# Kernel optimization log

Hardware: AMD Instinct MI355X
Metric: run time of the kernel (lower is better)

The kernel has to match this reference:

```python
import jax, jax.numpy as jnp
import numpy as np

D_MODEL = 16   # output feature dim of channel_proj
D_STATE = 8    # Mamba SSM state size
D_CONV = 2     # causal depthwise conv kernel size
D_INNER = 4    # expand * mamba_d_model = 2 * 2
DT_RANK = 1    # ceil(mamba_d_model / 16)


def setup_inputs() -> dict:
    key = jax.random.key(0)
    ks = jax.random.split(key, 10)
    B, W, P, T = 8, 16, 36, 2048
    s = 0.1
    raw_signals = jax.random.normal(ks[0], (B, W, P, 2, T), jnp.float32)
    in_proj_w = jax.random.normal(ks[1], (2 * D_INNER, 2), jnp.float32) * s
    conv_w = jax.random.normal(ks[2], (D_INNER, D_CONV), jnp.float32) * s
    conv_b = jax.random.normal(ks[3], (D_INNER,), jnp.float32) * s
    x_proj_w = jax.random.normal(ks[4], (DT_RANK + 2 * D_STATE, D_INNER), jnp.float32) * s
    dt_proj_w = jax.random.normal(ks[5], (D_INNER, DT_RANK), jnp.float32) * s
    dt_proj_b = jax.random.normal(ks[6], (D_INNER,), jnp.float32) * s
    # Standard S4D-real init: A_log = log(1..d_state) per inner channel
    A_log = jnp.log(jnp.tile(jnp.arange(1, D_STATE + 1, dtype=jnp.float32), (D_INNER, 1)))
    D_skip = jnp.ones((D_INNER,), jnp.float32)
    out_proj_w = jax.random.normal(ks[7], (2, D_INNER), jnp.float32) * s
    proj_w = jax.random.normal(ks[8], (D_MODEL, 2), jnp.float32) * s
    proj_b = jax.random.normal(ks[9], (D_MODEL,), jnp.float32) * s
    return dict(raw_signals=raw_signals, in_proj_w=in_proj_w, conv_w=conv_w,
                conv_b=conv_b, x_proj_w=x_proj_w, dt_proj_w=dt_proj_w,
                dt_proj_b=dt_proj_b, A_log=A_log, D_skip=D_skip,
                out_proj_w=out_proj_w, proj_w=proj_w, proj_b=proj_b)


def _mamba(u, in_proj_w, conv_w, conv_b, x_proj_w, dt_proj_w, dt_proj_b,
           A_log, D_skip, out_proj_w):
    # u: [N, L, 2] -> [N, L, 2]
    N, L, _ = u.shape
    xz = u @ in_proj_w.T                               # [N, L, 2*D_INNER]
    x, z = jnp.split(xz, 2, axis=-1)                   # each [N, L, D_INNER]
    # causal depthwise conv1d (kernel D_CONV, left-padded)
    xp = jnp.pad(x, ((0, 0), (D_CONV - 1, 0), (0, 0)))
    xc = sum(xp[:, k:k + L, :] * conv_w[:, k] for k in range(D_CONV)) + conv_b
    x = jax.nn.silu(xc)
    x_dbl = x @ x_proj_w.T                             # [N, L, DT_RANK + 2*D_STATE]
    dt, Bs, Cs = jnp.split(x_dbl, [DT_RANK, DT_RANK + D_STATE], axis=-1)
    dt = jax.nn.softplus(dt @ dt_proj_w.T + dt_proj_b)  # [N, L, D_INNER]
    A = -jnp.exp(A_log)                                # [D_INNER, D_STATE]

    def step(h, inp):
        dt_t, B_t, x_t, C_t = inp                      # [N,d], [N,s], [N,d], [N,s]
        dA = jnp.exp(dt_t[:, :, None] * A)             # [N, d, s]
        h = dA * h + (dt_t * x_t)[:, :, None] * B_t[:, None, :]
        y = jnp.einsum('nds,ns->nd', h, C_t)
        return h, y

    h0 = jnp.zeros((N, D_INNER, D_STATE), u.dtype)
    xs = (dt.transpose(1, 0, 2), Bs.transpose(1, 0, 2),
          x.transpose(1, 0, 2), Cs.transpose(1, 0, 2))
    _, ys = jax.lax.scan(step, h0, xs)                 # ys: [L, N, D_INNER]
    y = ys.transpose(1, 0, 2) + x * D_skip
    y = y * jax.nn.silu(z)
    return y @ out_proj_w.T                            # [N, L, 2]


def reference(raw_signals, in_proj_w, conv_w, conv_b, x_proj_w, dt_proj_w,
              dt_proj_b, A_log, D_skip, out_proj_w, proj_w, proj_b):
    B, W, P, C, T = raw_signals.shape
    # permute(0,1,3,2) per window + reshape(-1, T, C): all windows batched at once
    u = raw_signals.transpose(0, 1, 2, 4, 3).reshape(B * W * P, T, C)
    y = _mamba(u, in_proj_w, conv_w, conv_b, x_proj_w, dt_proj_w, dt_proj_b,
               A_log, D_skip, out_proj_w)              # [BWP, T, 2]
    feat = y.mean(axis=1)                              # [BWP, 2]
    proj = jax.nn.relu(feat @ proj_w.T + proj_b)       # [BWP, D_MODEL] (dropout=eval no-op)
    out = proj.reshape(B, W, P, D_MODEL).mean(axis=2)  # aggregate_internal=True
    return out                                         # [B, W, D_MODEL]
```

## Files before the change

kernel.cpp:

```cpp
#include <hip/hip_runtime.h>


#define T_LEN  2048
#define N_SEQ  4608
#define SPB    2
#define TC     32
#define NCH    (T_LEN / TC)
#define LOG2E  1.4426950408889634f
#define LN2    0.6931471805599453f

__device__ __forceinline__ float fexp2(float x){ return __builtin_amdgcn_exp2f(x); }
__device__ __forceinline__ float frcp (float x){ return __builtin_amdgcn_rcpf(x); }
__device__ __forceinline__ float flog2(float x){ return __builtin_amdgcn_logf(x); }
__device__ __forceinline__ float silu_f(float v){ return v * frcp(1.0f + fexp2(v * -LOG2E)); }

__global__ __launch_bounds__(64, 4) void mamba_feat_kernel(
    const float* __restrict__ raw,
    const float* __restrict__ in_proj_w,
    const float* __restrict__ conv_w,
    const float* __restrict__ conv_b,
    const float* __restrict__ x_proj_w,
    const float* __restrict__ dt_proj_w,
    const float* __restrict__ dt_proj_b,
    const float* __restrict__ A_log,
    const float* __restrict__ D_skip,
    const float* __restrict__ out_proj_w,
    float* __restrict__ feat)
{
    __shared__ __attribute__((aligned(16))) float rec[SPB * TC * 32];

    const int j   = threadIdx.x;
    const int seq = j >> 5;
    const int tt  = j & 31;
    const int d2  = (j & 31) >> 3;
    const int s2  = j & 7;

    float wi[8][2];
#pragma unroll
    for (int r = 0; r < 8; ++r){ wi[r][0] = in_proj_w[r*2]; wi[r][1] = in_proj_w[r*2+1]; }
    float cw0[4], cw1[4], cb[4], dtw[4], dtb[4], op0[4], op1[4], op0D[4], op1D[4];
#pragma unroll
    for (int d = 0; d < 4; ++d){
        cw0[d] = conv_w[d*2]; cw1[d] = conv_w[d*2+1]; cb[d] = conv_b[d];
        dtw[d] = dt_proj_w[d]; dtb[d] = dt_proj_b[d];
        op0[d] = out_proj_w[d]; op1[d] = out_proj_w[4+d];
        float Dk = D_skip[d];
        op0D[d] = op0[d] * Dk; op1D[d] = op1[d] * Dk;
    }
    float xw[17][4];
#pragma unroll
    for (int r = 0; r < 17; ++r)
#pragma unroll
        for (int d = 0; d < 4; ++d) xw[r][d] = x_proj_w[r*4 + d];
    const float A2l = -fexp2(A_log[d2*8 + s2] * LOG2E) * LOG2E;

    const int n = blockIdx.x * SPB + seq;
    const float* u0base = raw + (size_t)n * 2 * T_LEN;
    const float* u1base = u0base + T_LEN;

    const int sbase = seq * (TC * 32);
    const int sl_dt = d2 >> 1,        in_dt = (d2 & 1) * 2;
    const int sl_bc = 2 + (s2 >> 1),  in_bc = (s2 & 1) * 2;
    int odt[8], obc[8], og[8];
#pragma unroll
    for (int k2 = 0; k2 < 8; ++k2){
        odt[k2] = sbase + ((sl_dt ^ k2) << 2) + in_dt;
        obc[k2] = sbase + ((sl_bc ^ k2) << 2) + in_bc;
        og [k2] = sbase + ((6     ^ k2) << 2) + d2;
    }

    float h = 0.f, q = 0.f, sk0 = 0.f, sk1 = 0.f;

    float cu0 = u0base[tt], cu1 = u1base[tt];
    float pu0 = (tt > 0) ? u0base[tt-1] : 0.f;
    float pu1 = (tt > 0) ? u1base[tt-1] : 0.f;
    float nu0 = 0.f, nu1 = 0.f, np0 = 0.f, np1 = 0.f;

    for (int c = 0; c < NCH; ++c){
        float x[4], g[4];
#pragma unroll
        for (int d = 0; d < 4; ++d){
            float xr = fmaf(cu0, wi[d][0],   cu1 * wi[d][1]);
            float xp = fmaf(pu0, wi[d][0],   pu1 * wi[d][1]);
            float zr = fmaf(cu0, wi[4+d][0], cu1 * wi[4+d][1]);
            float xc = fmaf(xp, cw0[d], fmaf(xr, cw1[d], cb[d]));
            x[d] = silu_f(xc);
            g[d] = silu_f(zr);
        }
        float dtr = 0.f;
#pragma unroll
        for (int d = 0; d < 4; ++d) dtr = fmaf(x[d], xw[0][d], dtr);
        float Bv[8], Cv[8];
#pragma unroll
        for (int s = 0; s < 8; ++s){
            float b  = x[0] * xw[1+s][0];
            float cc = x[0] * xw[9+s][0];
#pragma unroll
            for (int d = 1; d < 4; ++d){
                b  = fmaf(x[d], xw[1+s][d], b);
                cc = fmaf(x[d], xw[9+s][d], cc);
            }
            Bv[s] = b; Cv[s] = cc;
        }
        float dt[4], dtx[4];
#pragma unroll
        for (int d = 0; d < 4; ++d){
            float v = fmaf(dtr, dtw[d], dtb[d]);
            dt[d]  = LN2 * flog2(1.0f + fexp2(v * LOG2E));
            dtx[d] = dt[d] * x[d];
        }
#pragma unroll
        for (int d = 0; d < 4; ++d){
            float gx = g[d] * x[d];
            sk0 = fmaf(gx, op0D[d], sk0);
            sk1 = fmaf(gx, op1D[d], sk1);
        }
        {
            const int rb = seq*(TC*32) + tt*32;
            const int tk = tt & 7;
            *(float4*)&rec[rb + ((0^tk)<<2)] = make_float4(dt[0], dtx[0], dt[1], dtx[1]);
            *(float4*)&rec[rb + ((1^tk)<<2)] = make_float4(dt[2], dtx[2], dt[3], dtx[3]);
            *(float4*)&rec[rb + ((2^tk)<<2)] = make_float4(Bv[0], Cv[0], Bv[1], Cv[1]);
            *(float4*)&rec[rb + ((3^tk)<<2)] = make_float4(Bv[2], Cv[2], Bv[3], Cv[3]);
            *(float4*)&rec[rb + ((4^tk)<<2)] = make_float4(Bv[4], Cv[4], Bv[5], Cv[5]);
            *(float4*)&rec[rb + ((5^tk)<<2)] = make_float4(Bv[6], Cv[6], Bv[7], Cv[7]);
            *(float4*)&rec[rb + ((6^tk)<<2)] = make_float4(g[0], g[1], g[2], g[3]);
        }
        __syncthreads();

        if (c + 1 < NCH){
            const int t = (c+1)*TC + tt;
            nu0 = u0base[t];   nu1 = u1base[t];
            np0 = u0base[t-1]; np1 = u1base[t-1];
        }

#pragma unroll
        for (int st = 0; st < TC; ++st){
            const int k2 = st & 7;
            const int tb = st * 32;
            const float2 ddx = *(const float2*)&rec[tb + odt[k2]];
            const float2 bc  = *(const float2*)&rec[tb + obc[k2]];
            const float  gt  = rec[tb + og[k2]];
            const float dA = fexp2(ddx.x * A2l);
            h = fmaf(dA, h, ddx.y * bc.x);
            q = fmaf(h, bc.y * gt, q);
        }
        __syncthreads();

        cu0 = nu0; cu1 = nu1; pu0 = np0; pu1 = np1;
    }

    float v0 = fmaf(q, op0[d2], sk0);
    float v1 = fmaf(q, op1[d2], sk1);
#pragma unroll
    for (int m = 16; m >= 1; m >>= 1){
        v0 += __shfl_xor(v0, m, 64);
        v1 += __shfl_xor(v1, m, 64);
    }
    if ((j & 31) == 0){
        feat[(size_t)n*2    ] = v0 * (1.0f / T_LEN);
        feat[(size_t)n*2 + 1] = v1 * (1.0f / T_LEN);
    }
}

__global__ void proj_kernel(const float* __restrict__ feat,
                            const float* __restrict__ pw,
                            const float* __restrict__ pb,
                            float* __restrict__ out)
{
    const int tid = blockIdx.x * blockDim.x + threadIdx.x;
    const int grp = tid >> 4;
    const int m   = tid & 15;
    const float w0 = pw[m*2], w1 = pw[m*2+1], b = pb[m];
    const float* f = feat + (size_t)grp * 36 * 2;
    float acc = 0.f;
#pragma unroll
    for (int p = 0; p < 36; ++p){
        float v = fmaf(f[p*2], w0, fmaf(f[p*2+1], w1, b));
        acc += fmaxf(v, 0.f);
    }
    out[tid] = acc * (1.0f / 36.0f);
}

extern "C" void kernel_launch(void* const* d_in, const int* in_sizes, int n_in,
                              void* d_out, int out_size, void* d_ws, size_t ws_size,
                              hipStream_t stream)
{
    (void)in_sizes; (void)n_in; (void)out_size; (void)ws_size;
    const float* raw        = (const float*)d_in[0];
    const float* in_proj_w  = (const float*)d_in[1];
    const float* conv_w     = (const float*)d_in[2];
    const float* conv_b     = (const float*)d_in[3];
    const float* x_proj_w   = (const float*)d_in[4];
    const float* dt_proj_w  = (const float*)d_in[5];
    const float* dt_proj_b  = (const float*)d_in[6];
    const float* A_log      = (const float*)d_in[7];
    const float* D_skip     = (const float*)d_in[8];
    const float* out_proj_w = (const float*)d_in[9];
    const float* proj_w     = (const float*)d_in[10];
    const float* proj_b     = (const float*)d_in[11];

    float* feat = (float*)d_ws;

    mamba_feat_kernel<<<dim3(N_SEQ / SPB), dim3(64), 0, stream>>>(
        raw, in_proj_w, conv_w, conv_b, x_proj_w, dt_proj_w, dt_proj_b,
        A_log, D_skip, out_proj_w, feat);

    proj_kernel<<<dim3(8), dim3(256), 0, stream>>>(feat, proj_w, proj_b, (float*)d_out);
}
```

Baseline: 161.3 us.

## Split the sequence scan into two time halves with a linear-recurrence combine

The per-sequence selective scan is split across two blocks along time. The second half runs from a zero state and also accumulates the cumulative decay product weighted by C*gate, so its missing contribution from the first half's final state can be added afterwards. A new combine kernel merges the partial sums, which doubles the grid and shortens each block's serial chain. The second half does extra multiplies per step, and the change adds a kernel launch plus workspace traffic.

```diff
diff --git a/kernel.cpp b/kernel.cpp
--- a/kernel.cpp
+++ b/kernel.cpp
@@ -5,7 +5,9 @@
 #define N_SEQ  4608
 #define SPB    2
 #define TC     32
-#define NCH    (T_LEN / TC)
+#define TSPLIT 2
+#define TH     (T_LEN / TSPLIT)
+#define NCHH   (TH / TC)
 #define LOG2E  1.4426950408889634f
 #define LN2    0.6931471805599453f
 
@@ -14,7 +16,7 @@
 __device__ __forceinline__ float flog2(float x){ return __builtin_amdgcn_logf(x); }
 __device__ __forceinline__ float silu_f(float v){ return v * frcp(1.0f + fexp2(v * -LOG2E)); }
 
-__global__ __launch_bounds__(64, 4) void mamba_feat_kernel(
+__global__ __launch_bounds__(64, 4) void mamba_half_kernel(
     const float* __restrict__ raw,
     const float* __restrict__ in_proj_w,
     const float* __restrict__ conv_w,
@@ -25,15 +27,19 @@
     const float* __restrict__ A_log,
     const float* __restrict__ D_skip,
     const float* __restrict__ out_proj_w,
-    float* __restrict__ feat)
+    float* __restrict__ H0,
+    float* __restrict__ W1,
+    float* __restrict__ QR)
 {
     __shared__ __attribute__((aligned(16))) float rec[SPB * TC * 32];
 
-    const int j   = threadIdx.x;
-    const int seq = j >> 5;
-    const int tt  = j & 31;
-    const int d2  = (j & 31) >> 3;
-    const int s2  = j & 7;
+    const int j    = threadIdx.x;
+    const int seq  = j >> 5;
+    const int tt   = j & 31;
+    const int d2   = (j & 31) >> 3;
+    const int s2   = j & 7;
+    const int half = blockIdx.y;
+    const int t0   = half * TH;
 
     float wi[8][2];
 #pragma unroll
@@ -70,13 +76,15 @@
     }
 
     float h = 0.f, q = 0.f, sk0 = 0.f, sk1 = 0.f;
-
-    float cu0 = u0base[tt], cu1 = u1base[tt];
-    float pu0 = (tt > 0) ? u0base[tt-1] : 0.f;
-    float pu1 = (tt > 0) ? u1base[tt-1] : 0.f;
+    float p = 1.f, w = 0.f;
+
+    const int tg0 = t0 + tt;
+    float cu0 = u0base[tg0], cu1 = u1base[tg0];
+    float pu0 = (tg0 > 0) ? u0base[tg0-1] : 0.f;
+    float pu1 = (tg0 > 0) ? u1base[tg0-1] : 0.f;
     float nu0 = 0.f, nu1 = 0.f, np0 = 0.f, np1 = 0.f;
 
-    for (int c = 0; c < NCH; ++c){
+    for (int c = 0; c < NCHH; ++c){
         float x[4], g[4];
 #pragma unroll
         for (int d = 0; d < 4; ++d){
@@ -128,27 +136,47 @@
         }
         __syncthreads();
 
-        if (c + 1 < NCH){
-            const int t = (c+1)*TC + tt;
+        if (c + 1 < NCHH){
+            const int t = t0 + (c+1)*TC + tt;
             nu0 = u0base[t];   nu1 = u1base[t];
             np0 = u0base[t-1]; np1 = u1base[t-1];
         }
 
-#pragma unroll
-        for (int st = 0; st < TC; ++st){
-            const int k2 = st & 7;
-            const int tb = st * 32;
-            const float2 ddx = *(const float2*)&rec[tb + odt[k2]];
-            const float2 bc  = *(const float2*)&rec[tb + obc[k2]];
-            const float  gt  = rec[tb + og[k2]];
-            const float dA = fexp2(ddx.x * A2l);
-            h = fmaf(dA, h, ddx.y * bc.x);
-            q = fmaf(h, bc.y * gt, q);
+        if (half == 0){
+#pragma unroll
+            for (int st = 0; st < TC; ++st){
+                const int k2 = st & 7;
+                const int tb = st * 32;
+                const float2 ddx = *(const float2*)&rec[tb + odt[k2]];
+                const float2 bc  = *(const float2*)&rec[tb + obc[k2]];
+                const float  gt  = rec[tb + og[k2]];
+                const float dA = fexp2(ddx.x * A2l);
+                h = fmaf(dA, h, ddx.y * bc.x);
+                q = fmaf(h, bc.y * gt, q);
+            }
+        } else {
+#pragma unroll
+            for (int st = 0; st < TC; ++st){
+                const int k2 = st & 7;
+                const int tb = st * 32;
+                const float2 ddx = *(const float2*)&rec[tb + odt[k2]];
+                const float2 bc  = *(const float2*)&rec[tb + obc[k2]];
+                const float  gt  = rec[tb + og[k2]];
+                const float dA = fexp2(ddx.x * A2l);
+                const float cg = bc.y * gt;
+                h = fmaf(dA, h, ddx.y * bc.x);
+                q = fmaf(h, cg, q);
+                p *= dA;
+                w = fmaf(p, cg, w);
+            }
         }
         __syncthreads();
 
         cu0 = nu0; cu1 = nu1; pu0 = np0; pu1 = np1;
     }
+
+    if (half == 0) H0[(size_t)n*32 + (j & 31)] = h;
+    else           W1[(size_t)n*32 + (j & 31)] = w;
 
     float v0 = fmaf(q, op0[d2], sk0);
     float v1 = fmaf(q, op1[d2], sk1);
@@ -158,8 +186,35 @@
         v1 += __shfl_xor(v1, m, 64);
     }
     if ((j & 31) == 0){
-        feat[(size_t)n*2    ] = v0 * (1.0f / T_LEN);
-        feat[(size_t)n*2 + 1] = v1 * (1.0f / T_LEN);
+        QR[(size_t)n*4 + half*2    ] = v0;
+        QR[(size_t)n*4 + half*2 + 1] = v1;
+    }
+}
+
+__global__ void combine_kernel(const float* __restrict__ H0,
+                               const float* __restrict__ W1,
+                               const float* __restrict__ QR,
+                               const float* __restrict__ opw,
+                               float* __restrict__ feat)
+{
+    const int j   = threadIdx.x;
+    const int seq = j >> 5;
+    const int k   = j & 31;
+    const int d2  = k >> 3;
+    const int n   = blockIdx.x * 8 + seq;
+    const float val = H0[(size_t)n*32 + k] * W1[(size_t)n*32 + k];
+    float v0 = val * opw[d2];
+    float v1 = val * opw[4 + d2];
+#pragma unroll
+    for (int m = 16; m >= 1; m >>= 1){
+        v0 += __shfl_xor(v0, m, 64);
+        v1 += __shfl_xor(v1, m, 64);
+    }
+    if (k == 0){
+        const float q00 = QR[(size_t)n*4+0], q01 = QR[(size_t)n*4+1];
+        const float q10 = QR[(size_t)n*4+2], q11 = QR[(size_t)n*4+3];
+        feat[(size_t)n*2    ] = (q00 + q10 + v0) * (1.0f / T_LEN);
+        feat[(size_t)n*2 + 1] = (q01 + q11 + v1) * (1.0f / T_LEN);
     }
 }
 
@@ -200,11 +255,16 @@
     const float* proj_w     = (const float*)d_in[10];
     const float* proj_b     = (const float*)d_in[11];
 
-    float* feat = (float*)d_ws;
-
-    mamba_feat_kernel<<<dim3(N_SEQ / SPB), dim3(64), 0, stream>>>(
+    float* H0   = (float*)d_ws;
+    float* W1   = H0 + (size_t)N_SEQ*32;
+    float* QR   = W1 + (size_t)N_SEQ*32;
+    float* feat = QR + (size_t)N_SEQ*4;
+
+    mamba_half_kernel<<<dim3(N_SEQ / SPB, TSPLIT), dim3(64), 0, stream>>>(
         raw, in_proj_w, conv_w, conv_b, x_proj_w, dt_proj_w, dt_proj_b,
-        A_log, D_skip, out_proj_w, feat);
+        A_log, D_skip, out_proj_w, H0, W1, QR);
+
+    combine_kernel<<<dim3(N_SEQ / 8), dim3(256), 0, stream>>>(H0, W1, QR, out_proj_w, feat);
 
     proj_kernel<<<dim3(8), dim3(256), 0, stream>>>(feat, proj_w, proj_b, (float*)d_out);
 }
```

After: 169.2 us. +4.9%, slower.

## Use 64-step chunks with planar padded LDS layout and vectorized scan reads

Applied to the files above, without the earlier changes.

The time chunk doubles from 32 to 64 steps, so each thread computes two timesteps per chunk and the number of barrier pairs is halved. The interleaved XOR-swizzled record buffer becomes separate planar arrays (dt/dtx, B/C, gate), one padded row per channel or state, so each scan step pair loads with float4/float2 reads from a contiguous row. The LOG2E scaling is folded into the dt projection weights, and the skip term is kept as per-channel sums that are combined once at the end. This costs more registers and LDS per block, which could lower occupancy or add bank conflicts on the write side.

```diff
diff --git a/kernel.cpp b/kernel.cpp
--- a/kernel.cpp
+++ b/kernel.cpp
@@ -4,10 +4,14 @@
 #define T_LEN  2048
 #define N_SEQ  4608
 #define SPB    2
-#define TC     32
+#define TC     64
 #define NCH    (T_LEN / TC)
 #define LOG2E  1.4426950408889634f
 #define LN2    0.6931471805599453f
+
+#define DDX_ROW 132
+#define BC_ROW  132
+#define G_ROW   66
 
 __device__ __forceinline__ float fexp2(float x){ return __builtin_amdgcn_exp2f(x); }
 __device__ __forceinline__ float frcp (float x){ return __builtin_amdgcn_rcpf(x); }
@@ -27,7 +31,9 @@
     const float* __restrict__ out_proj_w,
     float* __restrict__ feat)
 {
-    __shared__ __attribute__((aligned(16))) float rec[SPB * TC * 32];
+    __shared__ __attribute__((aligned(16))) float ddxP[SPB * 4 * DDX_ROW];
+    __shared__ __attribute__((aligned(16))) float bcP [SPB * 8 * BC_ROW];
+    __shared__ __attribute__((aligned(16))) float gP  [SPB * 4 * G_ROW];
 
     const int j   = threadIdx.x;
     const int seq = j >> 5;
@@ -38,11 +44,11 @@
     float wi[8][2];
 #pragma unroll
     for (int r = 0; r < 8; ++r){ wi[r][0] = in_proj_w[r*2]; wi[r][1] = in_proj_w[r*2+1]; }
-    float cw0[4], cw1[4], cb[4], dtw[4], dtb[4], op0[4], op1[4], op0D[4], op1D[4];
+    float cw0[4], cw1[4], cb[4], dtwL[4], dtbL[4], op0[4], op1[4], op0D[4], op1D[4];
 #pragma unroll
     for (int d = 0; d < 4; ++d){
         cw0[d] = conv_w[d*2]; cw1[d] = conv_w[d*2+1]; cb[d] = conv_b[d];
-        dtw[d] = dt_proj_w[d]; dtb[d] = dt_proj_b[d];
+        dtwL[d] = dt_proj_w[d] * LOG2E; dtbL[d] = dt_proj_b[d] * LOG2E;
         op0[d] = out_proj_w[d]; op1[d] = out_proj_w[4+d];
         float Dk = D_skip[d];
         op0D[d] = op0[d] * Dk; op1D[d] = op1[d] * Dk;
@@ -52,106 +58,113 @@
     for (int r = 0; r < 17; ++r)
 #pragma unroll
         for (int d = 0; d < 4; ++d) xw[r][d] = x_proj_w[r*4 + d];
-    const float A2l = -fexp2(A_log[d2*8 + s2] * LOG2E) * LOG2E;
+    const float Al = -fexp2(A_log[d2*8 + s2] * LOG2E);
 
     const int n = blockIdx.x * SPB + seq;
     const float* u0base = raw + (size_t)n * 2 * T_LEN;
     const float* u1base = u0base + T_LEN;
 
-    const int sbase = seq * (TC * 32);
-    const int sl_dt = d2 >> 1,        in_dt = (d2 & 1) * 2;
-    const int sl_bc = 2 + (s2 >> 1),  in_bc = (s2 & 1) * 2;
-    int odt[8], obc[8], og[8];
-#pragma unroll
-    for (int k2 = 0; k2 < 8; ++k2){
-        odt[k2] = sbase + ((sl_dt ^ k2) << 2) + in_dt;
-        obc[k2] = sbase + ((sl_bc ^ k2) << 2) + in_bc;
-        og [k2] = sbase + ((6     ^ k2) << 2) + d2;
-    }
-
-    float h = 0.f, q = 0.f, sk0 = 0.f, sk1 = 0.f;
-
-    float cu0 = u0base[tt], cu1 = u1base[tt];
-    float pu0 = (tt > 0) ? u0base[tt-1] : 0.f;
-    float pu1 = (tt > 0) ? u1base[tt-1] : 0.f;
-    float nu0 = 0.f, nu1 = 0.f, np0 = 0.f, np1 = 0.f;
+    const int wdd = seq*4*DDX_ROW;
+    const int wbc = seq*8*BC_ROW;
+    const int wg  = seq*4*G_ROW;
+    const int rdd = seq*4*DDX_ROW + d2*DDX_ROW;
+    const int rbc = seq*8*BC_ROW  + s2*BC_ROW;
+    const int rg  = seq*4*G_ROW   + d2*G_ROW;
+
+    float h = 0.f, q = 0.f;
+    float sgx[4] = {0.f, 0.f, 0.f, 0.f};
+
+    float cu0[2], cu1[2], pu0[2], pu1[2];
+    float nu0[2], nu1[2], np0[2], np1[2];
+#pragma unroll
+    for (int p = 0; p < 2; ++p){
+        const int t = p*32 + tt;
+        cu0[p] = u0base[t];  cu1[p] = u1base[t];
+        pu0[p] = (t > 0) ? u0base[t-1] : 0.f;
+        pu1[p] = (t > 0) ? u1base[t-1] : 0.f;
+    }
 
     for (int c = 0; c < NCH; ++c){
-        float x[4], g[4];
-#pragma unroll
-        for (int d = 0; d < 4; ++d){
-            float xr = fmaf(cu0, wi[d][0],   cu1 * wi[d][1]);
-            float xp = fmaf(pu0, wi[d][0],   pu1 * wi[d][1]);
-            float zr = fmaf(cu0, wi[4+d][0], cu1 * wi[4+d][1]);
-            float xc = fmaf(xp, cw0[d], fmaf(xr, cw1[d], cb[d]));
-            x[d] = silu_f(xc);
-            g[d] = silu_f(zr);
-        }
-        float dtr = 0.f;
-#pragma unroll
-        for (int d = 0; d < 4; ++d) dtr = fmaf(x[d], xw[0][d], dtr);
-        float Bv[8], Cv[8];
-#pragma unroll
-        for (int s = 0; s < 8; ++s){
-            float b  = x[0] * xw[1+s][0];
-            float cc = x[0] * xw[9+s][0];
-#pragma unroll
-            for (int d = 1; d < 4; ++d){
-                b  = fmaf(x[d], xw[1+s][d], b);
-                cc = fmaf(x[d], xw[9+s][d], cc);
-            }
-            Bv[s] = b; Cv[s] = cc;
-        }
-        float dt[4], dtx[4];
-#pragma unroll
-        for (int d = 0; d < 4; ++d){
-            float v = fmaf(dtr, dtw[d], dtb[d]);
-            dt[d]  = LN2 * flog2(1.0f + fexp2(v * LOG2E));
-            dtx[d] = dt[d] * x[d];
-        }
-#pragma unroll
-        for (int d = 0; d < 4; ++d){
-            float gx = g[d] * x[d];
-            sk0 = fmaf(gx, op0D[d], sk0);
-            sk1 = fmaf(gx, op1D[d], sk1);
-        }
-        {
-            const int rb = seq*(TC*32) + tt*32;
-            const int tk = tt & 7;
-            *(float4*)&rec[rb + ((0^tk)<<2)] = make_float4(dt[0], dtx[0], dt[1], dtx[1]);
-            *(float4*)&rec[rb + ((1^tk)<<2)] = make_float4(dt[2], dtx[2], dt[3], dtx[3]);
-            *(float4*)&rec[rb + ((2^tk)<<2)] = make_float4(Bv[0], Cv[0], Bv[1], Cv[1]);
-            *(float4*)&rec[rb + ((3^tk)<<2)] = make_float4(Bv[2], Cv[2], Bv[3], Cv[3]);
-            *(float4*)&rec[rb + ((4^tk)<<2)] = make_float4(Bv[4], Cv[4], Bv[5], Cv[5]);
-            *(float4*)&rec[rb + ((5^tk)<<2)] = make_float4(Bv[6], Cv[6], Bv[7], Cv[7]);
-            *(float4*)&rec[rb + ((6^tk)<<2)] = make_float4(g[0], g[1], g[2], g[3]);
+#pragma unroll
+        for (int p = 0; p < 2; ++p){
+            const float a0 = cu0[p], a1 = cu1[p], b0 = pu0[p], b1 = pu1[p];
+            const int tpos = p*32 + tt;
+            float x[4], g[4];
+#pragma unroll
+            for (int d = 0; d < 4; ++d){
+                float xr = fmaf(a0, wi[d][0],   a1 * wi[d][1]);
+                float xp = fmaf(b0, wi[d][0],   b1 * wi[d][1]);
+                float zr = fmaf(a0, wi[4+d][0], a1 * wi[4+d][1]);
+                float xc = fmaf(xp, cw0[d], fmaf(xr, cw1[d], cb[d]));
+                x[d] = silu_f(xc);
+                g[d] = silu_f(zr);
+            }
+            float dtr = 0.f;
+#pragma unroll
+            for (int d = 0; d < 4; ++d) dtr = fmaf(x[d], xw[0][d], dtr);
+            float Bv[8], Cv[8];
+#pragma unroll
+            for (int s = 0; s < 8; ++s){
+                float b  = x[0] * xw[1+s][0];
+                float cc = x[0] * xw[9+s][0];
+#pragma unroll
+                for (int d = 1; d < 4; ++d){
+                    b  = fmaf(x[d], xw[1+s][d], b);
+                    cc = fmaf(x[d], xw[9+s][d], cc);
+                }
+                Bv[s] = b; Cv[s] = cc;
+            }
+#pragma unroll
+            for (int d = 0; d < 4; ++d){
+                float vl  = fmaf(dtr, dtwL[d], dtbL[d]);
+                float dts = flog2(1.0f + fexp2(vl));
+                float dtx = (LN2 * dts) * x[d];
+                *(float2*)&ddxP[wdd + d*DDX_ROW + tpos*2] = make_float2(dts, dtx);
+                sgx[d] = fmaf(g[d], x[d], sgx[d]);
+                gP[wg + d*G_ROW + tpos] = g[d];
+            }
+#pragma unroll
+            for (int s = 0; s < 8; ++s)
+                *(float2*)&bcP[wbc + s*BC_ROW + tpos*2] = make_float2(Bv[s], Cv[s]);
         }
         __syncthreads();
 
         if (c + 1 < NCH){
-            const int t = (c+1)*TC + tt;
-            nu0 = u0base[t];   nu1 = u1base[t];
-            np0 = u0base[t-1]; np1 = u1base[t-1];
-        }
-
-#pragma unroll
-        for (int st = 0; st < TC; ++st){
-            const int k2 = st & 7;
-            const int tb = st * 32;
-            const float2 ddx = *(const float2*)&rec[tb + odt[k2]];
-            const float2 bc  = *(const float2*)&rec[tb + obc[k2]];
-            const float  gt  = rec[tb + og[k2]];
-            const float dA = fexp2(ddx.x * A2l);
-            h = fmaf(dA, h, ddx.y * bc.x);
-            q = fmaf(h, bc.y * gt, q);
+#pragma unroll
+            for (int p = 0; p < 2; ++p){
+                const int t = (c+1)*TC + p*32 + tt;
+                nu0[p] = u0base[t];   nu1[p] = u1base[t];
+                np0[p] = u0base[t-1]; np1[p] = u1base[t-1];
+            }
+        }
+
+#pragma unroll
+        for (int tp = 0; tp < TC/2; ++tp){
+            const float4 dx = *(const float4*)&ddxP[rdd + tp*4];
+            const float4 bc = *(const float4*)&bcP [rbc + tp*4];
+            const float2 gg = *(const float2*)&gP  [rg  + tp*2];
+            const float dA0 = fexp2(dx.x * Al);
+            h = fmaf(dA0, h, dx.y * bc.x);
+            q = fmaf(h, bc.y * gg.x, q);
+            const float dA1 = fexp2(dx.z * Al);
+            h = fmaf(dA1, h, dx.w * bc.z);
+            q = fmaf(h, bc.w * gg.y, q);
         }
         __syncthreads();
 
-        cu0 = nu0; cu1 = nu1; pu0 = np0; pu1 = np1;
-    }
-
-    float v0 = fmaf(q, op0[d2], sk0);
-    float v1 = fmaf(q, op1[d2], sk1);
+#pragma unroll
+        for (int p = 0; p < 2; ++p){
+            cu0[p] = nu0[p]; cu1[p] = nu1[p]; pu0[p] = np0[p]; pu1[p] = np1[p];
+        }
+    }
+
+    float v0 = q * op0[d2];
+    float v1 = q * op1[d2];
+#pragma unroll
+    for (int d = 0; d < 4; ++d){
+        v0 = fmaf(sgx[d], op0D[d], v0);
+        v1 = fmaf(sgx[d], op1D[d], v1);
+    }
 #pragma unroll
     for (int m = 16; m >= 1; m >>= 1){
         v0 += __shfl_xor(v0, m, 64);
```

Result: slower. 168.7 us (+4.6%).
